# Kernel tuning notes

Hardware: AMD Instinct MI355X
Metric: run time of the kernel (lower is better)

Reference implementation:

```python
import jax, jax.numpy as jnp
import numpy as np

NUM_HEADS = 16


def setup_inputs() -> dict:
    key = jax.random.key(0)
    k1, k2, k3, k4 = jax.random.split(key, 4)
    in_dim, out_dim = 1024, 1024
    x = jax.random.normal(k1, (4, 2048, in_dim), dtype=jnp.float32)
    # nn.Linear weights stored as [out, in]; we keep that convention.
    s = 1.0 / np.sqrt(in_dim)
    Wq = jax.random.uniform(k2, (out_dim, in_dim), jnp.float32, -s, s)
    Wk = jax.random.uniform(k3, (out_dim, in_dim), jnp.float32, -s, s)
    Wv = jax.random.uniform(k4, (out_dim, in_dim), jnp.float32, -s, s)
    return {"x": x, "Wq": Wq, "Wk": Wk, "Wv": Wv}


def reference(x, Wq, Wk, Wv):
    b, n, _ = x.shape
    out_dim = Wq.shape[0]
    h = NUM_HEADS
    d = out_dim // h  # head_dim

    def split_heads(t):  # [b,n,out] -> [b,h,n,d]
        return t.reshape(b, n, h, d).transpose(0, 2, 1, 3)

    q = split_heads(x @ Wq.T)
    k = split_heads(x @ Wk.T)
    v = split_heads(x @ Wv.T)

    scores = jnp.einsum("bhqd,bhkd->bhqk", q, k) / jnp.sqrt(jnp.float32(d))
    causal = jnp.tril(jnp.ones((n, n), dtype=bool))
    scores = jnp.where(causal, scores, -jnp.inf)
    attn = jax.nn.softmax(scores, axis=-1)
    out = jnp.einsum("bhqk,bhkd->bhqd", attn, v)
    return out.transpose(0, 2, 1, 3).reshape(b, n, out_dim)
```

## Files before the change

### kernel.cpp

```cpp
#include <hip/hip_runtime.h>

typedef __attribute__((ext_vector_type(8))) short short8;
typedef __attribute__((ext_vector_type(4))) short short4v;
typedef __attribute__((ext_vector_type(4))) float floatx4;
typedef __attribute__((ext_vector_type(16))) float floatx16;

#define GLOBAL_AS __attribute__((address_space(1)))
#define LDS_AS __attribute__((address_space(3)))

__device__ __forceinline__ short f2bs(float f) {
    union { float f; unsigned u; } v; v.f = f;
    unsigned r = v.u + 0x7fffu + ((v.u >> 16) & 1u);
    return (short)(r >> 16);
}

#if __has_builtin(__builtin_amdgcn_cvt_pk_bf16_f32)
typedef __attribute__((ext_vector_type(2))) __bf16 bf16x2;
__device__ __forceinline__ unsigned pk2(float a, float b) {
    union { bf16x2 v; unsigned u; } u;
    u.v = __builtin_amdgcn_cvt_pk_bf16_f32(a, b);
    return u.u;
}
#else
__device__ __forceinline__ unsigned pk2(float a, float b) {
    union { float f; unsigned u; } x, y; x.f = a; y.f = b;
    return ((y.u + 0x8000u) & 0xffff0000u) | ((x.u + 0x8000u) >> 16);
}
#endif

__global__ __launch_bounds__(256) void cast_all(const float* __restrict__ x,
                                                const float* __restrict__ Wq,
                                                const float* __restrict__ Wk,
                                                const float* __restrict__ Wv,
                                                short* __restrict__ xb,
                                                short* __restrict__ wb) {
    int b = blockIdx.x;
    int t = threadIdx.x;
    const float* src;
    short* dst;
    int idx;
    if (b < 8192) {
        src = x; dst = xb; idx = b * 1024 + t * 4;
    } else {
        int r = b - 8192;
        int wz = r >> 10;
        src = (wz == 0) ? Wq : (wz == 1) ? Wk : Wv;
        dst = wb + wz * (1 << 20);
        idx = (r & 1023) * 1024 + t * 4;
    }
    float4 v = *(const float4*)(src + idx);
    short4v o;
    o.x = f2bs(v.x); o.y = f2bs(v.y); o.z = f2bs(v.z); o.w = f2bs(v.w);
    *(short4v*)(dst + idx) = o;
}

__global__ __launch_bounds__(256) void qkv_gemm(const short* __restrict__ xb,
                                                const short* __restrict__ wb,
                                                short* __restrict__ qout,
                                                short* __restrict__ kout,
                                                short* __restrict__ vtout) {
    __shared__ short As[128 * 64];
    __shared__ short Bs[128 * 64];
    const int K = 1024;
    int tid = threadIdx.x;
    int lane = tid & 63;
    int wid = tid >> 6;
    int quad = lane >> 4;
    int l16 = lane & 15;
    int wm = (wid >> 1) * 64;
    int wn = (wid & 1) * 64;
    int bm = blockIdx.x * 128;
    int bn = blockIdx.y * 128;
    const short* W = wb + (size_t)blockIdx.z * K * 1024;
    bool vpath = (blockIdx.z == 2);

    floatx4 acc[4][4];
#pragma unroll
    for (int i = 0; i < 4; i++)
#pragma unroll
        for (int j = 0; j < 4; j++) acc[i][j] = (floatx4){0.f, 0.f, 0.f, 0.f};

    int srow = tid >> 3;
    int ssw = ((tid & 7) ^ (srow & 7)) * 8;

    for (int kk = 0; kk < K; kk += 64) {
        __syncthreads();
#pragma unroll
        for (int l = 0; l < 4; l++) {
            const short* g = xb + (size_t)(bm + srow + l * 32) * K + kk + ssw;
            __builtin_amdgcn_global_load_lds((const GLOBAL_AS void*)g,
                                             (LDS_AS void*)(As + tid * 8 + l * 2048), 16, 0, 0);
        }
#pragma unroll
        for (int l = 0; l < 4; l++) {
            const short* g = W + (size_t)(bn + srow + l * 32) * K + kk + ssw;
            __builtin_amdgcn_global_load_lds((const GLOBAL_AS void*)g,
                                             (LDS_AS void*)(Bs + tid * 8 + l * 2048), 16, 0, 0);
        }
        __syncthreads();

        if (vpath) {
#pragma unroll
            for (int s = 0; s < 2; s++) {
                int slot = ((s * 4 + quad) ^ (l16 & 7)) * 8;
                short8 af[4], bf[4];
#pragma unroll
                for (int i = 0; i < 4; i++)
                    af[i] = *(const short8*)(As + (wm + i * 16 + l16) * 64 + slot);
#pragma unroll
                for (int j = 0; j < 4; j++)
                    bf[j] = *(const short8*)(Bs + (wn + j * 16 + l16) * 64 + slot);
#pragma unroll
                for (int i = 0; i < 4; i++)
#pragma unroll
                    for (int j = 0; j < 4; j++)
                        acc[i][j] = __builtin_amdgcn_mfma_f32_16x16x32_bf16(af[i], bf[j], acc[i][j], 0, 0, 0);
            }
        } else {
#pragma unroll
            for (int s = 0; s < 2; s++) {
                int slot = ((s * 4 + quad) ^ (l16 & 7)) * 8;
                short8 af[4], bf[4];
#pragma unroll
                for (int i = 0; i < 4; i++)
                    af[i] = *(const short8*)(As + (wm + i * 16 + l16) * 64 + slot);
#pragma unroll
                for (int j = 0; j < 4; j++)
                    bf[j] = *(const short8*)(Bs + (wn + j * 16 + l16) * 64 + slot);
#pragma unroll
                for (int i = 0; i < 4; i++)
#pragma unroll
                    for (int j = 0; j < 4; j++)
                        acc[i][j] = __builtin_amdgcn_mfma_f32_16x16x32_bf16(bf[j], af[i], acc[i][j], 0, 0, 0);
            }
        }
    }

    if (vpath) {
#pragma unroll
        for (int i = 0; i < 4; i++) {
#pragma unroll
            for (int j = 0; j < 4; j++) {
                int m = bm + wm + i * 16 + quad * 4;
                int c = bn + wn + j * 16 + l16;
                int b = m >> 11, nn = m & 2047, h = c >> 6, dd = c & 63;
                int2 wv;
                wv.x = pk2(acc[i][j][0], acc[i][j][1]);
                wv.y = pk2(acc[i][j][2], acc[i][j][3]);
                *(int2*)(vtout + ((size_t)(b * 16 + h) * 64 + dd) * 2048 + nn) = wv;
            }
        }
    } else {
        short* dst = (blockIdx.z == 0) ? qout : kout;
        float qs = (blockIdx.z == 0) ? 0.180336881f : 1.0f;
#pragma unroll
        for (int i = 0; i < 4; i++) {
#pragma unroll
            for (int j = 0; j < 4; j++) {
                int seq = bm + wm + i * 16 + l16;
                int ob = bn + wn + j * 16 + quad * 4;
                int b = seq >> 11, nn = seq & 2047, h = ob >> 6, dd = ob & 63;
                int2 wv;
                wv.x = pk2(acc[i][j][0] * qs, acc[i][j][1] * qs);
                wv.y = pk2(acc[i][j][2] * qs, acc[i][j][3] * qs);
                *(int2*)(dst + ((size_t)(b * 16 + h) * 2048 + nn) * 64 + dd) = wv;
            }
        }
    }
}

__global__ __launch_bounds__(256, 2) void attn(const short* __restrict__ q,
                                               const short* __restrict__ k,
                                               const short* __restrict__ vt,
                                               float* __restrict__ out) {
    __shared__ short Ks[128 * 64];
    __shared__ short Vs[64 * 128];
    __shared__ short Ps[4 * 32 * 136];

    int tid = threadIdx.x;
    int lane = tid & 63;
    int wid = tid >> 6;
    int l32 = lane & 31;
    int half = lane >> 5;

    int flat = blockIdx.x;
    int xcd = flat & 7;
    int slot = flat >> 3;
    int bh = xcd * 8 + (slot >> 3);
    int qx = slot & 7;
    int b = bh >> 4, h = bh & 15;

    const short* qp = q + (size_t)(b * 16 + h) * 2048 * 64;
    const short* kp = k + (size_t)(b * 16 + h) * 2048 * 64;
    const short* vp = vt + (size_t)(b * 16 + h) * 64 * 2048;

    int krow = tid >> 3;
    int ksw = ((tid & 7) ^ (krow & 7)) * 8;
    int vd = tid >> 4;
    int vc = tid & 15;
    int vsw = ((vc & 8) | ((vc ^ vd) & 7)) * 8;

    short* pw = Ps + wid * (32 * 136);

    for (int phase = 0; phase < 2; phase++) {
        int qt = (phase == 0) ? qx : (15 - qx);
        int qbase = qt * 128;
        int qrow_w = qbase + wid * 32;
        int qlane = qrow_w + l32;

        short8 qf[4];
#pragma unroll
        for (int s = 0; s < 4; s++)
            qf[s] = *(const short8*)(qp + (size_t)qlane * 64 + s * 16 + half * 8);

        floatx16 oacc[2];
#pragma unroll
        for (int nt = 0; nt < 2; nt++)
#pragma unroll
            for (int e = 0; e < 16; e++) oacc[nt][e] = 0.f;
        float rs = 0.f;

        int ntiles = qt + 1;
        for (int t = 0; t < ntiles; t++) {
            int kvb = t * 128;
            __syncthreads();
#pragma unroll
            for (int l = 0; l < 4; l++) {
                const short* g = kp + (size_t)(kvb + krow + l * 32) * 64 + ksw;
                __builtin_amdgcn_global_load_lds((const GLOBAL_AS void*)g,
                                                 (LDS_AS void*)(Ks + tid * 8 + l * 2048), 16, 0, 0);
            }
#pragma unroll
            for (int l = 0; l < 4; l++) {
                const short* g = vp + (size_t)(vd + l * 16) * 2048 + kvb + vsw;
                __builtin_amdgcn_global_load_lds((const GLOBAL_AS void*)g,
                                                 (LDS_AS void*)(Vs + tid * 8 + l * 2048), 16, 0, 0);
            }
            __syncthreads();

            floatx16 sacc[4];
#pragma unroll
            for (int kb = 0; kb < 4; kb++)
#pragma unroll
                for (int e = 0; e < 16; e++) sacc[kb][e] = 0.f;
#pragma unroll
            for (int s = 0; s < 4; s++) {
#pragma unroll
                for (int kb = 0; kb < 4; kb++) {
                    int key = kb * 32 + l32;
                    int c = s * 2 + half;
                    short8 kf = *(const short8*)(Ks + key * 64 + ((c ^ (key & 7)) * 8));
                    sacc[kb] = __builtin_amdgcn_mfma_f32_32x32x16_bf16(kf, qf[s], sacc[kb], 0, 0, 0);
                }
            }

            bool diag = (t == ntiles - 1);
#pragma unroll
            for (int kb = 0; kb < 4; kb++) {
#pragma unroll
                for (int e = 0; e < 16; e++) {
                    float p = __builtin_amdgcn_exp2f(sacc[kb][e]);
                    if (diag) {
                        int key = kvb + kb * 32 + (e & 3) + 8 * (e >> 2) + 4 * half;
                        p = (key > qlane) ? 0.f : p;
                    }
                    sacc[kb][e] = p;
                    rs += p;
                }
#pragma unroll
                for (int g = 0; g < 4; g++) {
                    int2 wv;
                    wv.x = pk2(sacc[kb][4 * g], sacc[kb][4 * g + 1]);
                    wv.y = pk2(sacc[kb][4 * g + 2], sacc[kb][4 * g + 3]);
                    *(int2*)(pw + l32 * 136 + kb * 32 + g * 8 + 4 * half) = wv;
                }
            }
            __threadfence_block();

#pragma unroll
            for (int s = 0; s < 8; s++) {
                short8 pf = *(const short8*)(pw + l32 * 136 + s * 16 + half * 8);
#pragma unroll
                for (int nt = 0; nt < 2; nt++) {
                    int d = nt * 32 + l32;
                    int c = s * 2 + half;
                    int sl = (c & 8) | ((c ^ (d & 7)) & 7);
                    short8 vf = *(const short8*)(Vs + d * 128 + sl * 8);
                    oacc[nt] = __builtin_amdgcn_mfma_f32_32x32x16_bf16(vf, pf, oacc[nt], 0, 0, 0);
                }
            }
        }

        float tot = rs + __shfl_xor(rs, 32);
        float inv = 1.0f / tot;
        float* orow = out + ((size_t)b * 2048 + qlane) * 1024 + h * 64;
#pragma unroll
        for (int nt = 0; nt < 2; nt++) {
#pragma unroll
            for (int g = 0; g < 4; g++) {
                float4 o4;
                o4.x = oacc[nt][4 * g + 0] * inv;
                o4.y = oacc[nt][4 * g + 1] * inv;
                o4.z = oacc[nt][4 * g + 2] * inv;
                o4.w = oacc[nt][4 * g + 3] * inv;
                *(float4*)(orow + nt * 32 + 8 * g + 4 * half) = o4;
            }
        }
    }
}

extern "C" void kernel_launch(void* const* d_in, const int* in_sizes, int n_in,
                              void* d_out, int out_size, void* d_ws, size_t ws_size,
                              hipStream_t stream) {
    const float* x = (const float*)d_in[0];
    const float* Wq = (const float*)d_in[1];
    const float* Wk = (const float*)d_in[2];
    const float* Wv = (const float*)d_in[3];
    float* out = (float*)d_out;
    char* ws = (char*)d_ws;

    short* xb = (short*)ws;
    short* wb = (short*)(ws + (16u << 20));
    short* qb = (short*)(ws + (22u << 20));
    short* kb = (short*)(ws + (38u << 20));
    short* vtb = (short*)(ws + (54u << 20));

    cast_all<<<8192 + 3 * 1024, 256, 0, stream>>>(x, Wq, Wk, Wv, xb, wb);
    qkv_gemm<<<dim3(64, 8, 3), 256, 0, stream>>>(xb, wb, qb, kb, vtb);
    attn<<<512, 256, 0, stream>>>(qb, kb, vtb, out);
}
```

Baseline: 211.2 us.

## Halve attention P staging buffer to allow three blocks per CU; simplify QKV GEMM

The attention kernel now writes the softmaxed P tile to LDS in two 64-key chunks instead of one 128-key buffer. This halves the Ps shared buffer, and launch bounds are raised to 3 blocks per CU to gain occupancy. The QKV GEMM drops its separate operand-swapped path for Q/K and uses one MFMA ordering, so Q/K outputs are now written as scalar bf16 stores, which may cost store bandwidth. The chunking adds an extra fence per chunk, and the higher occupancy target may force register spills.

```diff
diff --git a/kernel.cpp b/kernel.cpp
--- a/kernel.cpp
+++ b/kernel.cpp
@@ -72,7 +72,6 @@
     int bm = blockIdx.x * 128;
     int bn = blockIdx.y * 128;
     const short* W = wb + (size_t)blockIdx.z * K * 1024;
-    bool vpath = (blockIdx.z == 2);
 
     floatx4 acc[4][4];
 #pragma unroll
@@ -99,44 +98,25 @@
         }
         __syncthreads();
 
-        if (vpath) {
-#pragma unroll
-            for (int s = 0; s < 2; s++) {
-                int slot = ((s * 4 + quad) ^ (l16 & 7)) * 8;
-                short8 af[4], bf[4];
-#pragma unroll
-                for (int i = 0; i < 4; i++)
-                    af[i] = *(const short8*)(As + (wm + i * 16 + l16) * 64 + slot);
+#pragma unroll
+        for (int s = 0; s < 2; s++) {
+            int slot = ((s * 4 + quad) ^ (l16 & 7)) * 8;
+            short8 af[4], bf[4];
+#pragma unroll
+            for (int i = 0; i < 4; i++)
+                af[i] = *(const short8*)(As + (wm + i * 16 + l16) * 64 + slot);
+#pragma unroll
+            for (int j = 0; j < 4; j++)
+                bf[j] = *(const short8*)(Bs + (wn + j * 16 + l16) * 64 + slot);
+#pragma unroll
+            for (int i = 0; i < 4; i++)
 #pragma unroll
                 for (int j = 0; j < 4; j++)
-                    bf[j] = *(const short8*)(Bs + (wn + j * 16 + l16) * 64 + slot);
-#pragma unroll
-                for (int i = 0; i < 4; i++)
-#pragma unroll
-                    for (int j = 0; j < 4; j++)
-                        acc[i][j] = __builtin_amdgcn_mfma_f32_16x16x32_bf16(af[i], bf[j], acc[i][j], 0, 0, 0);
-            }
-        } else {
-#pragma unroll
-            for (int s = 0; s < 2; s++) {
-                int slot = ((s * 4 + quad) ^ (l16 & 7)) * 8;
-                short8 af[4], bf[4];
-#pragma unroll
-                for (int i = 0; i < 4; i++)
-                    af[i] = *(const short8*)(As + (wm + i * 16 + l16) * 64 + slot);
-#pragma unroll
-                for (int j = 0; j < 4; j++)
-                    bf[j] = *(const short8*)(Bs + (wn + j * 16 + l16) * 64 + slot);
-#pragma unroll
-                for (int i = 0; i < 4; i++)
-#pragma unroll
-                    for (int j = 0; j < 4; j++)
-                        acc[i][j] = __builtin_amdgcn_mfma_f32_16x16x32_bf16(bf[j], af[i], acc[i][j], 0, 0, 0);
-            }
+                    acc[i][j] = __builtin_amdgcn_mfma_f32_16x16x32_bf16(af[i], bf[j], acc[i][j], 0, 0, 0);
         }
     }
 
-    if (vpath) {
+    if (blockIdx.z == 2) {
 #pragma unroll
         for (int i = 0; i < 4; i++) {
 #pragma unroll
@@ -157,25 +137,25 @@
         for (int i = 0; i < 4; i++) {
 #pragma unroll
             for (int j = 0; j < 4; j++) {
-                int seq = bm + wm + i * 16 + l16;
-                int ob = bn + wn + j * 16 + quad * 4;
-                int b = seq >> 11, nn = seq & 2047, h = ob >> 6, dd = ob & 63;
-                int2 wv;
-                wv.x = pk2(acc[i][j][0] * qs, acc[i][j][1] * qs);
-                wv.y = pk2(acc[i][j][2] * qs, acc[i][j][3] * qs);
-                *(int2*)(dst + ((size_t)(b * 16 + h) * 2048 + nn) * 64 + dd) = wv;
+#pragma unroll
+                for (int r = 0; r < 4; r++) {
+                    int m = bm + wm + i * 16 + quad * 4 + r;
+                    int c = bn + wn + j * 16 + l16;
+                    dst[((size_t)((m >> 11) * 16 + (c >> 6)) * 2048 + (m & 2047)) * 64 + (c & 63)] =
+                        f2bs(acc[i][j][r] * qs);
+                }
             }
         }
     }
 }
 
-__global__ __launch_bounds__(256, 2) void attn(const short* __restrict__ q,
+__global__ __launch_bounds__(256, 3) void attn(const short* __restrict__ q,
                                                const short* __restrict__ k,
                                                const short* __restrict__ vt,
                                                float* __restrict__ out) {
     __shared__ short Ks[128 * 64];
     __shared__ short Vs[64 * 128];
-    __shared__ short Ps[4 * 32 * 136];
+    __shared__ short Ps[4 * 32 * 72];
 
     int tid = threadIdx.x;
     int lane = tid & 63;
@@ -200,7 +180,7 @@
     int vc = tid & 15;
     int vsw = ((vc & 8) | ((vc ^ vd) & 7)) * 8;
 
-    short* pw = Ps + wid * (32 * 136);
+    short* pw = Ps + wid * (32 * 72);
 
     for (int phase = 0; phase < 2; phase++) {
         int qt = (phase == 0) ? qx : (15 - qx);
@@ -256,38 +236,44 @@
 
             bool diag = (t == ntiles - 1);
 #pragma unroll
-            for (int kb = 0; kb < 4; kb++) {
-#pragma unroll
-                for (int e = 0; e < 16; e++) {
-                    float p = __builtin_amdgcn_exp2f(sacc[kb][e]);
-                    if (diag) {
-                        int key = kvb + kb * 32 + (e & 3) + 8 * (e >> 2) + 4 * half;
-                        p = (key > qlane) ? 0.f : p;
+            for (int ch = 0; ch < 2; ch++) {
+#pragma unroll
+                for (int kbl = 0; kbl < 2; kbl++) {
+                    int kb = ch * 2 + kbl;
+#pragma unroll
+                    for (int e = 0; e < 16; e++) {
+                        float p = __builtin_amdgcn_exp2f(sacc[kb][e]);
+                        if (diag) {
+                            int key = kvb + kb * 32 + (e & 3) + 8 * (e >> 2) + 4 * half;
+                            p = (key > qlane) ? 0.f : p;
+                        }
+                        sacc[kb][e] = p;
+                        rs += p;
                     }
-                    sacc[kb][e] = p;
-                    rs += p;
+#pragma unroll
+                    for (int g = 0; g < 4; g++) {
+                        int2 wv;
+                        wv.x = pk2(sacc[kb][4 * g], sacc[kb][4 * g + 1]);
+                        wv.y = pk2(sacc[kb][4 * g + 2], sacc[kb][4 * g + 3]);
+                        *(int2*)(pw + l32 * 72 + kbl * 32 + g * 8 + 4 * half) = wv;
+                    }
                 }
-#pragma unroll
-                for (int g = 0; g < 4; g++) {
-                    int2 wv;
-                    wv.x = pk2(sacc[kb][4 * g], sacc[kb][4 * g + 1]);
-                    wv.y = pk2(sacc[kb][4 * g + 2], sacc[kb][4 * g + 3]);
-                    *(int2*)(pw + l32 * 136 + kb * 32 + g * 8 + 4 * half) = wv;
+                __threadfence_block();
+
+#pragma unroll
+                for (int sl = 0; sl < 4; sl++) {
+                    int s = ch * 4 + sl;
+                    short8 pf = *(const short8*)(pw + l32 * 72 + sl * 16 + half * 8);
+#pragma unroll
+                    for (int nt = 0; nt < 2; nt++) {
+                        int d = nt * 32 + l32;
+                        int c = s * 2 + half;
+                        int sl2 = (c & 8) | ((c ^ (d & 7)) & 7);
+                        short8 vf = *(const short8*)(Vs + d * 128 + sl2 * 8);
+                        oacc[nt] = __builtin_amdgcn_mfma_f32_32x32x16_bf16(vf, pf, oacc[nt], 0, 0, 0);
+                    }
                 }
-            }
-            __threadfence_block();
-
-#pragma unroll
-            for (int s = 0; s < 8; s++) {
-                short8 pf = *(const short8*)(pw + l32 * 136 + s * 16 + half * 8);
-#pragma unroll
-                for (int nt = 0; nt < 2; nt++) {
-                    int d = nt * 32 + l32;
-                    int c = s * 2 + half;
-                    int sl = (c & 8) | ((c ^ (d & 7)) & 7);
-                    short8 vf = *(const short8*)(Vs + d * 128 + sl * 8);
-                    oacc[nt] = __builtin_amdgcn_mfma_f32_32x32x16_bf16(vf, pf, oacc[nt], 0, 0, 0);
-                }
+                __threadfence_block();
             }
         }
 
```

After: 209.4 us. Within noise of the previous version (-0.8%).
